# Optimization experiments

Hardware: AMD Instinct MI355X
Metric: run time of the kernel (lower is better)

## Reference

```python
import jax, jax.numpy as jnp
import numpy as np

B, L, E, D1, D2 = 256, 128, 64, 512, 512


def setup_inputs() -> dict:
    key = jax.random.key(0)
    k1, k2, k3, kw = jax.random.split(key, 4)
    tensor1 = jax.random.normal(k1, (B, L, D1), dtype=jnp.float32)
    tensor2 = jax.random.normal(k2, (B, L, D2), dtype=jnp.float32)
    parameters_index = jax.random.randint(k3, (B,), 0, E, dtype=jnp.int32)
    # xavier_uniform with relu gain: gain*sqrt(6/(fan_in+fan_out)),
    # torch fan for [E,D1,D2]: fan_in = D1*D2, fan_out = E*D2
    gain = float(np.sqrt(2.0))
    bound = gain * float(np.sqrt(6.0 / (D1 * D2 + E * D2)))
    weights = jax.random.uniform(kw, (E, D1, D2), minval=-bound, maxval=bound, dtype=jnp.float32)
    return {"tensor1": tensor1, "tensor2": tensor2, "parameters_index": parameters_index, "weights": weights}


def reference(tensor1, tensor2, parameters_index, weights):
    # gather per-batch weight matrix [B, D1, D2], then bilinear form x1^T W x2
    w = weights[parameters_index]  # [B, D1, D2]
    # equals: sum over i,j of tensor1[b,l,i] * w[b,i,j] * tensor2[b,l,j] -> [B, L]
    return jnp.einsum('bli,bij,blj->bl', tensor1, w, tensor2)
```

## Files before the change

### kernel.cpp

```cpp
#include <hip/hip_runtime.h>
#include <stdint.h>

#define NB 256
#define NL 128
#define ND1 512
#define ND2 512

#define BN 128
#define BK 64
#define NKT (ND1 / BK)
#define LDST 72

typedef float float4_t __attribute__((ext_vector_type(4)));
typedef __bf16 bf16x8_t __attribute__((ext_vector_type(8)));
typedef unsigned short ushort4_t __attribute__((ext_vector_type(4)));
typedef unsigned short ushort8_t __attribute__((ext_vector_type(8)));

__device__ __forceinline__ unsigned short f2bf(float f) {
    unsigned int u = __float_as_uint(f);
    u += 0x7FFFu + ((u >> 16) & 1u);
    return (unsigned short)(u >> 16);
}

__global__ __launch_bounds__(256, 3) void pdot_kernel(
    const float* __restrict__ t1, const float* __restrict__ t2,
    const int* __restrict__ pidx, const float* __restrict__ wgt,
    float* __restrict__ out)
{
    __shared__ unsigned short sA[NL * LDST];
    __shared__ unsigned short sB[BN * LDST];

    const int g  = blockIdx.x;
    const int b  = g & (NB - 1);
    const int jt = g >> 8;
    const int j0 = jt * BN;

    const int t  = threadIdx.x;
    const int wv = t >> 6;
    const int ln = t & 63;
    const int nh = ln & 15;
    const int qd = ln >> 4;

    const int e = pidx[b];
    const float* t1p = t1  + (size_t)b * (NL * ND1);
    const float* t2p = t2  + (size_t)b * (NL * ND2) + j0;
    const float* wp  = wgt + (size_t)e * (ND1 * ND2) + j0;

    float4_t acc[2][8];
    #pragma unroll
    for (int i = 0; i < 2; ++i)
        #pragma unroll
        for (int j = 0; j < 8; ++j) {
            float4_t z = {0.f, 0.f, 0.f, 0.f};
            acc[i][j] = z;
        }

    const int a_m = t >> 4;
    const int a_k = (t & 15) * 4;
    const int w_n  = ((t >> 4) & 7) * 16 + (t & 15);
    const int w_k8 = (t >> 7) * 8;

    for (int kt = 0; kt < NKT; ++kt) {
        const int k0 = kt * BK;

        #pragma unroll
        for (int p = 0; p < 8; ++p) {
            const int m = p * 16 + a_m;
            float4_t v = *(const float4_t*)(t1p + (size_t)m * ND1 + (k0 + a_k));
            ushort4_t u;
            u.x = f2bf(v.x); u.y = f2bf(v.y); u.z = f2bf(v.z); u.w = f2bf(v.w);
            *(ushort4_t*)(&sA[m * LDST + a_k]) = u;
        }

        #pragma unroll
        for (int p = 0; p < 4; ++p) {
            const int kk = p * 16 + w_k8;
            const float* src = wp + (size_t)(k0 + kk) * ND2 + w_n;
            ushort8_t u;
            #pragma unroll
            for (int i = 0; i < 8; ++i)
                u[i] = f2bf(src[(size_t)i * ND2]);
            *(ushort8_t*)(&sB[w_n * LDST + kk]) = u;
        }

        __syncthreads();

        #pragma unroll
        for (int ks = 0; ks < 2; ++ks) {
            const int kf = ks * 32 + qd * 8;
            bf16x8_t af[2];
            bf16x8_t bfr[8];
            #pragma unroll
            for (int ms = 0; ms < 2; ++ms) {
                const int row = wv * 32 + ms * 16 + nh;
                af[ms] = __builtin_bit_cast(bf16x8_t, *(ushort8_t*)(&sA[row * LDST + kf]));
            }
            #pragma unroll
            for (int ns = 0; ns < 8; ++ns) {
                const int nr = ns * 16 + nh;
                bfr[ns] = __builtin_bit_cast(bf16x8_t, *(ushort8_t*)(&sB[nr * LDST + kf]));
            }
            #pragma unroll
            for (int ms = 0; ms < 2; ++ms)
                #pragma unroll
                for (int ns = 0; ns < 8; ++ns)
                    acc[ms][ns] = __builtin_amdgcn_mfma_f32_16x16x32_bf16(af[ms], bfr[ns], acc[ms][ns], 0, 0, 0);
        }

        __syncthreads();
    }

    #pragma unroll
    for (int ms = 0; ms < 2; ++ms) {
        #pragma unroll
        for (int r = 0; r < 4; ++r) {
            const int row = wv * 32 + ms * 16 + qd * 4 + r;
            float ps = 0.f;
            #pragma unroll
            for (int ns = 0; ns < 8; ++ns) {
                const float tv = t2p[(size_t)row * ND2 + ns * 16 + nh];
                ps += acc[ms][ns][r] * tv;
            }
            ps += __shfl_xor(ps, 1);
            ps += __shfl_xor(ps, 2);
            ps += __shfl_xor(ps, 4);
            ps += __shfl_xor(ps, 8);
            if (nh == 0) atomicAdd(&out[b * NL + row], ps);
        }
    }
}

extern "C" void kernel_launch(void* const* d_in, const int* in_sizes, int n_in,
                              void* d_out, int out_size, void* d_ws, size_t ws_size,
                              hipStream_t stream)
{
    const float* t1  = (const float*)d_in[0];
    const float* t2  = (const float*)d_in[1];
    const int* pidx  = (const int*)d_in[2];
    const float* wgt = (const float*)d_in[3];
    float* out = (float*)d_out;

    hipMemsetAsync(out, 0, (size_t)out_size * sizeof(float), stream);
    pdot_kernel<<<dim3(NB * (ND2 / BN)), dim3(256), 0, stream>>>(t1, t2, pidx, wgt, out);
}
```

Before: 244.3 us.

## Contract over D2 first so weight tiles load row-contiguous with float4

```diff
diff --git a/kernel.cpp b/kernel.cpp
--- a/kernel.cpp
+++ b/kernel.cpp
@@ -6,9 +6,9 @@
 #define ND1 512
 #define ND2 512
 
-#define BN 128
+#define BI 128
 #define BK 64
-#define NKT (ND1 / BK)
+#define NKT (ND2 / BK)
 #define LDST 72
 
 typedef float float4_t __attribute__((ext_vector_type(4)));
@@ -22,18 +22,18 @@
     return (unsigned short)(u >> 16);
 }
 
-__global__ __launch_bounds__(256, 3) void pdot_kernel(
+__global__ __launch_bounds__(256, 4) void pdot_kernel(
     const float* __restrict__ t1, const float* __restrict__ t2,
     const int* __restrict__ pidx, const float* __restrict__ wgt,
     float* __restrict__ out)
 {
     __shared__ unsigned short sA[NL * LDST];
-    __shared__ unsigned short sB[BN * LDST];
+    __shared__ unsigned short sB[BI * LDST];
 
     const int g  = blockIdx.x;
     const int b  = g & (NB - 1);
-    const int jt = g >> 8;
-    const int j0 = jt * BN;
+    const int it = g >> 8;
+    const int i0 = it * BI;
 
     const int t  = threadIdx.x;
     const int wv = t >> 6;
@@ -42,9 +42,9 @@
     const int qd = ln >> 4;
 
     const int e = pidx[b];
-    const float* t1p = t1  + (size_t)b * (NL * ND1);
-    const float* t2p = t2  + (size_t)b * (NL * ND2) + j0;
-    const float* wp  = wgt + (size_t)e * (ND1 * ND2) + j0;
+    const float* aPtr  = t2  + (size_t)b * (NL * ND2);
+    const float* bPtr  = wgt + (size_t)e * (ND1 * ND2) + (size_t)i0 * ND2;
+    const float* t1p   = t1  + (size_t)b * (NL * ND1) + i0;
 
     float4_t acc[2][8];
     #pragma unroll
@@ -55,32 +55,22 @@
             acc[i][j] = z;
         }
 
-    const int a_m = t >> 4;
-    const int a_k = (t & 15) * 4;
-    const int w_n  = ((t >> 4) & 7) * 16 + (t & 15);
-    const int w_k8 = (t >> 7) * 8;
+    const int s_row = t >> 4;
+    const int s_kq  = (t & 15) * 4;
 
     for (int kt = 0; kt < NKT; ++kt) {
         const int k0 = kt * BK;
 
         #pragma unroll
         for (int p = 0; p < 8; ++p) {
-            const int m = p * 16 + a_m;
-            float4_t v = *(const float4_t*)(t1p + (size_t)m * ND1 + (k0 + a_k));
-            ushort4_t u;
-            u.x = f2bf(v.x); u.y = f2bf(v.y); u.z = f2bf(v.z); u.w = f2bf(v.w);
-            *(ushort4_t*)(&sA[m * LDST + a_k]) = u;
-        }
-
-        #pragma unroll
-        for (int p = 0; p < 4; ++p) {
-            const int kk = p * 16 + w_k8;
-            const float* src = wp + (size_t)(k0 + kk) * ND2 + w_n;
-            ushort8_t u;
-            #pragma unroll
-            for (int i = 0; i < 8; ++i)
-                u[i] = f2bf(src[(size_t)i * ND2]);
-            *(ushort8_t*)(&sB[w_n * LDST + kk]) = u;
+            const int row = p * 16 + s_row;
+            float4_t va = *(const float4_t*)(aPtr + (size_t)row * ND2 + (k0 + s_kq));
+            float4_t vb = *(const float4_t*)(bPtr + (size_t)row * ND2 + (k0 + s_kq));
+            ushort4_t ua, ub;
+            ua.x = f2bf(va.x); ua.y = f2bf(va.y); ua.z = f2bf(va.z); ua.w = f2bf(va.w);
+            ub.x = f2bf(vb.x); ub.y = f2bf(vb.y); ub.z = f2bf(vb.z); ub.w = f2bf(vb.w);
+            *(ushort4_t*)(&sA[row * LDST + s_kq]) = ua;
+            *(ushort4_t*)(&sB[row * LDST + s_kq]) = ub;
         }
 
         __syncthreads();
@@ -118,7 +108,7 @@
             float ps = 0.f;
             #pragma unroll
             for (int ns = 0; ns < 8; ++ns) {
-                const float tv = t2p[(size_t)row * ND2 + ns * 16 + nh];
+                const float tv = t1p[(size_t)row * ND1 + ns * 16 + nh];
                 ps += acc[ms][ns][r] * tv;
             }
             ps += __shfl_xor(ps, 1);
@@ -141,5 +131,5 @@
     float* out = (float*)d_out;
 
     hipMemsetAsync(out, 0, (size_t)out_size * sizeof(float), stream);
-    pdot_kernel<<<dim3(NB * (ND2 / BN)), dim3(256), 0, stream>>>(t1, t2, pidx, wgt, out);
+    pdot_kernel<<<dim3(NB * (ND1 / BI)), dim3(256), 0, stream>>>(t1, t2, pidx, wgt, out);
 }
```

Result: no change. 242.6 us (-0.7%).
